# Kernel tuning notes

Hardware: AMD Instinct MI355X
Metric: run time of the kernel (lower is better)

The kernel has to match this reference:

```python
import jax, jax.numpy as jnp
from jax import lax
import numpy as np

B, C, H, W = 4, 128, 160, 160
C2 = 2 * C          # dwconv / channel-attention width
FP_HID = 2 * C      # Feature_Pool ratio=2
CA_HID = C2 // 16   # Channel_Attention ratio=16


def setup_inputs() -> dict:
    key = jax.random.key(0)
    ks = jax.random.split(key, 20)
    s = lambda *sh: 0.02
    return {
        "RGB": jax.random.normal(ks[0], (B, C, H, W), jnp.float32),
        "T": jax.random.normal(ks[1], (B, C, H, W), jnp.float32),
        # Feature_Pool (shared module applied to both RGB and T)
        "fp_down_w": jax.random.normal(ks[2], (FP_HID, C), jnp.float32) * 0.02,
        "fp_down_b": jnp.zeros((FP_HID,), jnp.float32),
        "fp_up_w": jax.random.normal(ks[3], (C, FP_HID), jnp.float32) * 0.02,
        "fp_up_b": jnp.zeros((C,), jnp.float32),
        # dwconv: Conv2d(2c, 2c, k=7, pad=3, groups=c) -> weight [2c, 2, 7, 7]
        "dw_w": jax.random.normal(ks[4], (C2, 2, 7, 7), jnp.float32) * 0.02,
        "dw_b": jnp.zeros((C2,), jnp.float32),
        # Channel_Attention on 2c
        "ca_down_w": jax.random.normal(ks[5], (CA_HID, C2), jnp.float32) * 0.02,
        "ca_down_b": jnp.zeros((CA_HID,), jnp.float32),
        "ca_up_w": jax.random.normal(ks[6], (C2, CA_HID), jnp.float32) * 0.02,
        "ca_up_b": jnp.zeros((C2,), jnp.float32),
        # Spatial_Attention 1x1 convs (c -> 1), stored as [c] vectors + scalar bias
        "sr_w": jax.random.normal(ks[7], (C,), jnp.float32) * 0.02,
        "sr_b": jnp.zeros((1,), jnp.float32),
        "st_w": jax.random.normal(ks[8], (C,), jnp.float32) * 0.02,
        "st_b": jnp.zeros((1,), jnp.float32),
    }


def _feature_pool(x, dw, db, uw, ub):
    # AdaptiveAvgPool2d(1) -> Linear -> GELU(exact) -> Linear ; returns [b, c]
    y = jnp.mean(x, axis=(2, 3))
    y = jax.nn.gelu(y @ dw.T + db, approximate=False)
    return y @ uw.T + ub


def _channel_att(x, dw, db, uw, ub):
    # AdaptiveMaxPool2d(1) -> Linear -> GELU(exact) -> Linear ; returns [b, 2c, 1, 1]
    y = jnp.max(x, axis=(2, 3))
    y = jax.nn.gelu(y @ dw.T + db, approximate=False)
    y = y @ uw.T + ub
    return y[:, :, None, None]


def reference(RGB, T, fp_down_w, fp_down_b, fp_up_w, fp_up_b, dw_w, dw_b,
              ca_down_w, ca_down_b, ca_up_w, ca_up_b, sr_w, sr_b, st_w, st_b):
    b, c, h, w = RGB.shape
    rgb_y = _feature_pool(RGB, fp_down_w, fp_down_b, fp_up_w, fp_up_b)
    t_y = _feature_pool(T, fp_down_w, fp_down_b, fp_up_w, fp_up_b)
    rgb_y = rgb_y / jnp.linalg.norm(rgb_y, axis=1, keepdims=True)
    t_y = t_y / jnp.linalg.norm(t_y, axis=1, keepdims=True)
    # logits_per = c * rgb_y[b,c,1] @ t_y[b,1,c] -> [b, c, c]
    logits = c * rgb_y[:, :, None] * t_y[:, None, :]
    # Faithful to torch.diagonal default (dim1=0, dim2=1): result[j,k] = logits[k,k,j],
    # shape [c, min(b,c)] = [c, b]; then reshape to (b, c, 1, 1). Requires b <= c.
    diag = jnp.diagonal(logits, axis1=0, axis2=1)
    cross_gate = jax.nn.sigmoid(diag).reshape(b, c, 1, 1)
    add_gate = 1.0 - cross_gate

    New_RGB_e = RGB * cross_gate
    New_T_e = T * cross_gate
    New_RGB_c = RGB * add_gate
    New_T_c = T * add_gate

    x_cat_e = jnp.concatenate([New_RGB_e, New_T_e], axis=1)  # [b, 2c, h, w]
    dw_out = lax.conv_general_dilated(
        x_cat_e, dw_w, window_strides=(1, 1), padding=[(3, 3), (3, 3)],
        dimension_numbers=("NCHW", "OIHW", "NCHW"), feature_group_count=c,
    ) + dw_b[None, :, None, None]

    fuse_gate = jax.nn.sigmoid(_channel_att(dw_out, ca_down_w, ca_down_b, ca_up_w, ca_up_b))
    rgb_gate_e, t_gate_e = fuse_gate[:, :c], fuse_gate[:, c:]

    New_RGB = New_RGB_e * rgb_gate_e + New_RGB_c
    New_T = New_T_e * t_gate_e + New_T_c

    # 1x1 conv c->1 (with bias) for each stream
    f_r = jnp.einsum("bchw,c->bhw", New_RGB, sr_w)[:, None] + sr_b[0]  # [b,1,h,w]
    f_t = jnp.einsum("bchw,c->bhw", New_T, st_w)[:, None] + st_b[0]
    att = jax.nn.softmax(jnp.concatenate([f_r, f_t], axis=1), axis=1)  # [b,2,h,w]

    New_RGB = New_RGB * att[:, 0:1]
    New_T = New_T * att[:, 1:2]
    return New_RGB, New_T
```

## Files before the change

### kernel.cpp

```cpp
#include <hip/hip_runtime.h>
#include <hip/hip_fp16.h>
#include <cfloat>
#include <cmath>

#define HW 25600
#define WIDTH 160
#define NB 4
#define NC 128

typedef float f32x4 __attribute__((ext_vector_type(4)));

__device__ __forceinline__ float gelu_exact(float x) {
    return 0.5f * x * (1.f + erff(x * 0.70710678118654752f));
}
__device__ __forceinline__ float sigmoidf_(float x) {
    return 1.f / (1.f + expf(-x));
}

__device__ __forceinline__ unsigned pack_pkrtz(float a, float b) {
    return __builtin_bit_cast(unsigned, __builtin_amdgcn_cvt_pkrtz(a, b));
}
__device__ __forceinline__ __half2 u2h(unsigned u) {
    return __builtin_bit_cast(__half2, u);
}
__device__ __forceinline__ float h2sum(__half2 h) {
    return __half2float(__low2half(h)) + __half2float(__high2half(h));
}

__global__ __launch_bounds__(256) void pack_w_kernel(const float* __restrict__ dww,
                                                     unsigned* __restrict__ wpk) {
    int i = blockIdx.x * 256 + threadIdx.x;
    if (i >= 128 * 98) return;
    int g = i / 98; int r = i - g * 98;
    int ky = r / 14; int r2 = r - ky * 14;
    int oc = r2 / 7; int kx = r2 - oc * 7;
    int o = 2 * g + oc;
    float wa = dww[(o * 2 + 0) * 49 + ky * 7 + kx];
    float wb = dww[(o * 2 + 1) * 49 + ky * 7 + kx];
    wpk[i] = pack_pkrtz(wa, wb);
}

__global__ __launch_bounds__(256) void mean_kernel(const float* __restrict__ RGB,
                                                   const float* __restrict__ T,
                                                   float* __restrict__ means) {
    int p = blockIdx.x;
    const float* src = (p < 512) ? (RGB + (size_t)p * HW)
                                 : (T + (size_t)(p - 512) * HW);
    const float4* s4 = (const float4*)src;
    float s = 0.f;
    for (int i = threadIdx.x; i < HW / 4; i += 256) {
        float4 v = s4[i];
        s += (v.x + v.y) + (v.z + v.w);
    }
    for (int off = 32; off; off >>= 1) s += __shfl_down(s, off);
    __shared__ float r[4];
    if ((threadIdx.x & 63) == 0) r[threadIdx.x >> 6] = s;
    __syncthreads();
    if (threadIdx.x == 0) means[p] = (r[0] + r[1] + r[2] + r[3]) * (1.f / (float)HW);
}

__global__ __launch_bounds__(256) void mlp_kernel(const float* __restrict__ means,
                                                  const float* __restrict__ dww,
                                                  const float* __restrict__ dwb,
                                                  const float* __restrict__ uww,
                                                  const float* __restrict__ uwb,
                                                  float* __restrict__ ynorm) {
    int tb = blockIdx.x;
    int t = threadIdx.x;
    __shared__ float sm[128];
    __shared__ float sh[256];
    __shared__ float zz[256];
    __shared__ float r4[4];
    if (t < 128) sm[t] = means[tb * 128 + t];
    __syncthreads();
    float a = dwb[t];
    const float* wrow = dww + t * 128;
    for (int c = 0; c < 128; ++c) a += wrow[c] * sm[c];
    sh[t] = gelu_exact(a);
    __syncthreads();
    int c = t & 127, half = t >> 7;
    float z = 0.f;
    const float* urow = uww + c * 256 + half * 128;
    const float* hh = sh + half * 128;
    for (int j = 0; j < 128; ++j) z += urow[j] * hh[j];
    zz[t] = z;
    __syncthreads();
    float y = 0.f;
    if (t < 128) y = zz[t] + zz[t + 128] + uwb[t];
    float p = y * y;
    for (int off = 32; off; off >>= 1) p += __shfl_down(p, off);
    if ((t & 63) == 0) r4[t >> 6] = p;
    __syncthreads();
    float nrm = sqrtf(r4[0] + r4[1] + r4[2] + r4[3]);
    if (t < 128) ynorm[tb * 128 + t] = y / nrm;
}

#define TW2 166
#define THR 22
#define NYT 10
__global__ __launch_bounds__(256, 4) void conv_max_kernel(const float* __restrict__ RGB,
                                                          const float* __restrict__ T,
                                                          const unsigned* __restrict__ wpk,
                                                          const float* __restrict__ ynorm,
                                                          float* __restrict__ part) {
    int yt = blockIdx.x;
    int g  = blockIdx.y;
    int b  = blockIdx.z;
    int t  = threadIdx.x;
    __shared__ unsigned tile[THR * TW2];
    __shared__ float r0s[4], r1s[4];
    int ic0 = 2 * g;
    int c0 = ic0 & 127, c1 = (ic0 + 1) & 127;
    const float* base = (ic0 < 128) ? RGB : T;
    const float* plane0 = base + ((size_t)(b * 128 + c0)) * HW;
    const float* plane1 = base + ((size_t)(b * 128 + c1)) * HW;
    int i0 = b * 128 + c0, i1 = b * 128 + c1;
    int j0 = i0 & 3, k0 = i0 >> 2, j1 = i1 & 3, k1 = i1 >> 2;
    float gate0 = sigmoidf_(128.f * ynorm[j0 * 128 + j0] * ynorm[512 + j0 * 128 + k0]);
    float gate1 = sigmoidf_(128.f * ynorm[j1 * 128 + j1] * ynorm[512 + j1 * 128 + k1]);
    int y0 = yt * 16 - 3;
    for (int e = t; e < THR * TW2; e += 256) {
        int row = e / TW2;
        int col = e - row * TW2;
        int gy = y0 + row, gx = col - 3;
        float v0 = 0.f, v1 = 0.f;
        if (gy >= 0 && gy < 160 && gx >= 0 && gx < 160) {
            int off = gy * WIDTH + gx;
            v0 = plane0[off] * gate0;
            v1 = plane1[off] * gate1;
        }
        tile[e] = pack_pkrtz(v0, v1);
    }
    __syncthreads();
    int xs = (t & 15) * 10;
    int ys = t >> 4;
    __half2 A0 = u2h(0u), A1 = u2h(0u), A2 = u2h(0u), A3 = u2h(0u), A4 = u2h(0u);
    __half2 A5 = u2h(0u), A6 = u2h(0u), A7 = u2h(0u), A8 = u2h(0u), A9 = u2h(0u);
    __half2 B0 = u2h(0u), B1 = u2h(0u), B2 = u2h(0u), B3 = u2h(0u), B4 = u2h(0u);
    __half2 B5 = u2h(0u), B6 = u2h(0u), B7 = u2h(0u), B8 = u2h(0u), B9 = u2h(0u);
    const unsigned* wgp = wpk + g * 98;
    #pragma unroll 1
    for (int ky = 0; ky < 7; ++ky) {
        unsigned wk[14];
        #pragma unroll
        for (int j = 0; j < 14; ++j) wk[j] = wgp[ky * 14 + j];
        const uint2* tr2 = (const uint2*)(tile + (ys + ky) * TW2 + xs);
        unsigned win[16];
        #pragma unroll
        for (int j = 0; j < 8; ++j) {
            uint2 p = tr2[j];
            win[2 * j] = p.x;
            win[2 * j + 1] = p.y;
        }
        #pragma unroll
        for (int kx = 0; kx < 7; ++kx) {
            __half2 w0 = u2h(wk[kx]);
            __half2 w1 = u2h(wk[7 + kx]);
            __half2 v;
            v = u2h(win[kx + 0]); A0 = __hfma2(w0, v, A0); B0 = __hfma2(w1, v, B0);
            v = u2h(win[kx + 1]); A1 = __hfma2(w0, v, A1); B1 = __hfma2(w1, v, B1);
            v = u2h(win[kx + 2]); A2 = __hfma2(w0, v, A2); B2 = __hfma2(w1, v, B2);
            v = u2h(win[kx + 3]); A3 = __hfma2(w0, v, A3); B3 = __hfma2(w1, v, B3);
            v = u2h(win[kx + 4]); A4 = __hfma2(w0, v, A4); B4 = __hfma2(w1, v, B4);
            v = u2h(win[kx + 5]); A5 = __hfma2(w0, v, A5); B5 = __hfma2(w1, v, B5);
            v = u2h(win[kx + 6]); A6 = __hfma2(w0, v, A6); B6 = __hfma2(w1, v, B6);
            v = u2h(win[kx + 7]); A7 = __hfma2(w0, v, A7); B7 = __hfma2(w1, v, B7);
            v = u2h(win[kx + 8]); A8 = __hfma2(w0, v, A8); B8 = __hfma2(w1, v, B8);
            v = u2h(win[kx + 9]); A9 = __hfma2(w0, v, A9); B9 = __hfma2(w1, v, B9);
        }
    }
    float m0 = fmaxf(fmaxf(fmaxf(h2sum(A0), h2sum(A1)), fmaxf(h2sum(A2), h2sum(A3))),
                     fmaxf(fmaxf(h2sum(A4), h2sum(A5)),
                           fmaxf(fmaxf(h2sum(A6), h2sum(A7)), fmaxf(h2sum(A8), h2sum(A9)))));
    float m1 = fmaxf(fmaxf(fmaxf(h2sum(B0), h2sum(B1)), fmaxf(h2sum(B2), h2sum(B3))),
                     fmaxf(fmaxf(h2sum(B4), h2sum(B5)),
                           fmaxf(fmaxf(h2sum(B6), h2sum(B7)), fmaxf(h2sum(B8), h2sum(B9)))));
    for (int off = 32; off; off >>= 1) {
        m0 = fmaxf(m0, __shfl_down(m0, off));
        m1 = fmaxf(m1, __shfl_down(m1, off));
    }
    if ((t & 63) == 0) { r0s[t >> 6] = m0; r1s[t >> 6] = m1; }
    __syncthreads();
    if (t == 0) {
        m0 = fmaxf(fmaxf(r0s[0], r0s[1]), fmaxf(r0s[2], r0s[3]));
        m1 = fmaxf(fmaxf(r1s[0], r1s[1]), fmaxf(r1s[2], r1s[3]));
        int bb = ((b * 128 + g) * NYT + yt) * 2;
        part[bb] = m0;
        part[bb + 1] = m1;
    }
}

__global__ __launch_bounds__(256) void att_kernel(const float* __restrict__ ynorm,
                                                  const float* __restrict__ part,
                                                  const float* __restrict__ dwb,
                                                  const float* __restrict__ cdw,
                                                  const float* __restrict__ cdb,
                                                  const float* __restrict__ cuw,
                                                  const float* __restrict__ cub,
                                                  const float* __restrict__ srw,
                                                  const float* __restrict__ stw,
                                                  float* __restrict__ coefs) {
    int t = threadIdx.x;
    __shared__ float scg[512];
    __shared__ float smax[1024];
    __shared__ float sh2[64];
    __shared__ float sfg[1024];
    for (int idx = t; idx < 512; idx += 256) {
        int kk = idx >> 2, j = idx & 3;
        scg[idx] = sigmoidf_(128.f * ynorm[j * 128 + j] * ynorm[512 + j * 128 + kk]);
    }
    for (int idx = t; idx < 1024; idx += 256) {
        int b = idx >> 8, o = idx & 255;
        int gg = o >> 1, oc = o & 1;
        const float* pp = part + ((b * 128 + gg) * NYT) * 2 + oc;
        float m = pp[0];
        #pragma unroll
        for (int yt = 1; yt < NYT; ++yt) m = fmaxf(m, pp[yt * 2]);
        smax[idx] = m + dwb[o];
    }
    __syncthreads();
    if (t < 64) {
        int b = t >> 4, j = t & 15;
        float a = cdb[j];
        const float* wrow = cdw + j * 256;
        const float* mx = smax + b * 256;
        for (int o = 0; o < 256; ++o) a += wrow[o] * mx[o];
        sh2[t] = gelu_exact(a);
    }
    __syncthreads();
    for (int idx = t; idx < 1024; idx += 256) {
        int b = idx >> 8, o = idx & 255;
        float z = cub[o];
        const float* ur = cuw + o * 16;
        const float* hh = sh2 + b * 16;
        #pragma unroll
        for (int j = 0; j < 16; ++j) z += ur[j] * hh[j];
        sfg[idx] = sigmoidf_(z);
    }
    __syncthreads();
    for (int idx = t; idx < 512; idx += 256) {
        int b = idx >> 7, c = idx & 127;
        float cgv = scg[idx];
        float ar = cgv * sfg[b * 256 + c] + 1.f - cgv;
        float at = cgv * sfg[b * 256 + 128 + c] + 1.f - cgv;
        coefs[idx] = ar;
        coefs[512 + idx] = at;
        coefs[1024 + idx] = ar * srw[c];
        coefs[1536 + idx] = at * stw[c];
    }
}

__global__ __launch_bounds__(256) void fuse_kernel(const float* __restrict__ RGB,
                                                   const float* __restrict__ T,
                                                   const float* __restrict__ coefs,
                                                   const float* __restrict__ srb,
                                                   const float* __restrict__ stb,
                                                   float* __restrict__ out) {
    int b = blockIdx.y;
    int t = threadIdx.x;
    int w = t >> 6, lane = t & 63;
    int pix = blockIdx.x * 256 + lane * 4;
    __shared__ float sco[4][128];
    for (int i = t; i < 512; i += 256) {
        int a = i >> 7, c = i & 127;
        sco[a][c] = coefs[a * 512 + b * 128 + c];
    }
    __syncthreads();
    const float* rp = RGB + (size_t)b * NC * HW;
    const float* tp = T + (size_t)b * NC * HW;
    float4 df = make_float4(0.f, 0.f, 0.f, 0.f);
    for (int ci = 0; ci < 32; ++ci) {
        int c = w + ci * 4;
        size_t off = (size_t)c * HW + pix;
        float4 r = *(const float4*)(rp + off);
        float4 tv = *(const float4*)(tp + off);
        float wrc = sco[2][c], wtc = sco[3][c];
        df.x += r.x * wrc - tv.x * wtc;
        df.y += r.y * wrc - tv.y * wtc;
        df.z += r.z * wrc - tv.z * wtc;
        df.w += r.w * wrc - tv.w * wtc;
    }
    __shared__ float4 sdf[4][64];
    sdf[w][lane] = df;
    __syncthreads();
    float4 d0 = sdf[0][lane], d1 = sdf[1][lane], d2 = sdf[2][lane], d3 = sdf[3][lane];
    float bias = srb[0] - stb[0];
    float ax = sigmoidf_(d0.x + d1.x + d2.x + d3.x + bias);
    float ay = sigmoidf_(d0.y + d1.y + d2.y + d3.y + bias);
    float az = sigmoidf_(d0.z + d1.z + d2.z + d3.z + bias);
    float aw = sigmoidf_(d0.w + d1.w + d2.w + d3.w + bias);
    float* outR = out + (size_t)b * NC * HW;
    float* outT = out + (size_t)NB * NC * HW + (size_t)b * NC * HW;
    for (int ci = 0; ci < 32; ++ci) {
        int c = w + ci * 4;
        size_t off = (size_t)c * HW + pix;
        float4 r = *(const float4*)(rp + off);
        float4 tv = *(const float4*)(tp + off);
        float arc = sco[0][c], atc = sco[1][c];
        f32x4 o1, o2;
        o1.x = r.x * arc * ax;  o2.x = tv.x * atc * (1.f - ax);
        o1.y = r.y * arc * ay;  o2.y = tv.y * atc * (1.f - ay);
        o1.z = r.z * arc * az;  o2.z = tv.z * atc * (1.f - az);
        o1.w = r.w * arc * aw;  o2.w = tv.w * atc * (1.f - aw);
        __builtin_nontemporal_store(o1, (f32x4*)(outR + off));
        __builtin_nontemporal_store(o2, (f32x4*)(outT + off));
    }
}

extern "C" void kernel_launch(void* const* d_in, const int* in_sizes, int n_in,
                              void* d_out, int out_size, void* d_ws, size_t ws_size,
                              hipStream_t stream) {
    const float* RGB       = (const float*)d_in[0];
    const float* T         = (const float*)d_in[1];
    const float* fp_down_w = (const float*)d_in[2];
    const float* fp_down_b = (const float*)d_in[3];
    const float* fp_up_w   = (const float*)d_in[4];
    const float* fp_up_b   = (const float*)d_in[5];
    const float* dw_w      = (const float*)d_in[6];
    const float* dw_b      = (const float*)d_in[7];
    const float* ca_down_w = (const float*)d_in[8];
    const float* ca_down_b = (const float*)d_in[9];
    const float* ca_up_w   = (const float*)d_in[10];
    const float* ca_up_b   = (const float*)d_in[11];
    const float* sr_w      = (const float*)d_in[12];
    const float* sr_b      = (const float*)d_in[13];
    const float* st_w      = (const float*)d_in[14];
    const float* st_b      = (const float*)d_in[15];
    float* out = (float*)d_out;
    float* ws  = (float*)d_ws;

    unsigned* wpk = (unsigned*)(ws + 14336);
    pack_w_kernel<<<49, 256, 0, stream>>>(dw_w, wpk);
    mean_kernel<<<1024, 256, 0, stream>>>(RGB, T, ws);
    mlp_kernel<<<8, 256, 0, stream>>>(ws, fp_down_w, fp_down_b, fp_up_w, fp_up_b, ws + 1024);
    conv_max_kernel<<<dim3(NYT, 128, 4), 256, 0, stream>>>(RGB, T, wpk, ws + 1024, ws + 2048);
    att_kernel<<<1, 256, 0, stream>>>(ws + 1024, ws + 2048, dw_b, ca_down_w, ca_down_b,
                                      ca_up_w, ca_up_b, sr_w, st_w, ws + 12288);
    fuse_kernel<<<dim3(100, 4), 256, 0, stream>>>(RGB, T, ws + 12288, sr_b, st_b, out);
}
```

Before: 153.7 us.

## Keep fuse-kernel inputs in registers and use one pixel per lane

The fuse kernel now caches each thread's 32 RGB and 32 T values in registers during the reduction pass and reuses them for the output pass, so it no longer re-reads both inputs from global memory. Each lane now handles one pixel with scalar loads instead of four pixels with float4, and each wave owns a contiguous block of 32 channels. The grid grows from 100 to 400 blocks per batch, with a launch-bounds occupancy hint. The cost is higher register pressure and narrower scalar memory accesses instead of vector ones.

```diff
diff --git a/kernel.cpp b/kernel.cpp
--- a/kernel.cpp
+++ b/kernel.cpp
@@ -250,16 +250,16 @@
     }
 }
 
-__global__ __launch_bounds__(256) void fuse_kernel(const float* __restrict__ RGB,
-                                                   const float* __restrict__ T,
-                                                   const float* __restrict__ coefs,
-                                                   const float* __restrict__ srb,
-                                                   const float* __restrict__ stb,
-                                                   float* __restrict__ out) {
+__global__ __launch_bounds__(256, 4) void fuse_kernel(const float* __restrict__ RGB,
+                                                      const float* __restrict__ T,
+                                                      const float* __restrict__ coefs,
+                                                      const float* __restrict__ srb,
+                                                      const float* __restrict__ stb,
+                                                      float* __restrict__ out) {
     int b = blockIdx.y;
     int t = threadIdx.x;
     int w = t >> 6, lane = t & 63;
-    int pix = blockIdx.x * 256 + lane * 4;
+    int pix = blockIdx.x * 64 + lane;
     __shared__ float sco[4][128];
     for (int i = t; i < 512; i += 256) {
         int a = i >> 7, c = i & 127;
@@ -268,42 +268,30 @@
     __syncthreads();
     const float* rp = RGB + (size_t)b * NC * HW;
     const float* tp = T + (size_t)b * NC * HW;
-    float4 df = make_float4(0.f, 0.f, 0.f, 0.f);
+    float rv[32], tv[32];
+    float df = 0.f;
+    #pragma unroll
     for (int ci = 0; ci < 32; ++ci) {
-        int c = w + ci * 4;
+        int c = w * 32 + ci;
         size_t off = (size_t)c * HW + pix;
-        float4 r = *(const float4*)(rp + off);
-        float4 tv = *(const float4*)(tp + off);
-        float wrc = sco[2][c], wtc = sco[3][c];
-        df.x += r.x * wrc - tv.x * wtc;
-        df.y += r.y * wrc - tv.y * wtc;
-        df.z += r.z * wrc - tv.z * wtc;
-        df.w += r.w * wrc - tv.w * wtc;
-    }
-    __shared__ float4 sdf[4][64];
+        rv[ci] = rp[off];
+        tv[ci] = tp[off];
+        df += rv[ci] * sco[2][c] - tv[ci] * sco[3][c];
+    }
+    __shared__ float sdf[4][64];
     sdf[w][lane] = df;
     __syncthreads();
-    float4 d0 = sdf[0][lane], d1 = sdf[1][lane], d2 = sdf[2][lane], d3 = sdf[3][lane];
-    float bias = srb[0] - stb[0];
-    float ax = sigmoidf_(d0.x + d1.x + d2.x + d3.x + bias);
-    float ay = sigmoidf_(d0.y + d1.y + d2.y + d3.y + bias);
-    float az = sigmoidf_(d0.z + d1.z + d2.z + d3.z + bias);
-    float aw = sigmoidf_(d0.w + d1.w + d2.w + d3.w + bias);
+    float a = sigmoidf_(sdf[0][lane] + sdf[1][lane] + sdf[2][lane] + sdf[3][lane]
+                        + srb[0] - stb[0]);
+    float na = 1.f - a;
     float* outR = out + (size_t)b * NC * HW;
     float* outT = out + (size_t)NB * NC * HW + (size_t)b * NC * HW;
+    #pragma unroll
     for (int ci = 0; ci < 32; ++ci) {
-        int c = w + ci * 4;
+        int c = w * 32 + ci;
         size_t off = (size_t)c * HW + pix;
-        float4 r = *(const float4*)(rp + off);
-        float4 tv = *(const float4*)(tp + off);
-        float arc = sco[0][c], atc = sco[1][c];
-        f32x4 o1, o2;
-        o1.x = r.x * arc * ax;  o2.x = tv.x * atc * (1.f - ax);
-        o1.y = r.y * arc * ay;  o2.y = tv.y * atc * (1.f - ay);
-        o1.z = r.z * arc * az;  o2.z = tv.z * atc * (1.f - az);
-        o1.w = r.w * arc * aw;  o2.w = tv.w * atc * (1.f - aw);
-        __builtin_nontemporal_store(o1, (f32x4*)(outR + off));
-        __builtin_nontemporal_store(o2, (f32x4*)(outT + off));
+        __builtin_nontemporal_store(rv[ci] * sco[0][c] * a, outR + off);
+        __builtin_nontemporal_store(tv[ci] * sco[1][c] * na, outT + off);
     }
 }
 
@@ -336,5 +324,5 @@
     conv_max_kernel<<<dim3(NYT, 128, 4), 256, 0, stream>>>(RGB, T, wpk, ws + 1024, ws + 2048);
     att_kernel<<<1, 256, 0, stream>>>(ws + 1024, ws + 2048, dw_b, ca_down_w, ca_down_b,
                                       ca_up_w, ca_up_b, sr_w, st_w, ws + 12288);
-    fuse_kernel<<<dim3(100, 4), 256, 0, stream>>>(RGB, T, ws + 12288, sr_b, st_b, out);
-}
+    fuse_kernel<<<dim3(400, 4), 256, 0, stream>>>(RGB, T, ws + 12288, sr_b, st_b, out);
+}
```

Measured after the change: 150.4 us. -2.1%, faster.
